# Optimization experiments

Measured on AMD Instinct MI355X. Metric: run time of the kernel, lower is better.

The kernel has to match this reference:

```python
import jax, jax.numpy as jnp
import numpy as np

H = W = 2048
TANH_C = 1.1486328125  # probability-correction constant from the model
DEG2RAD = np.float32(np.pi / 180.0)

# Fire-spread direction angle (degrees, East=0, counterclockwise) from the
# neighbor at 3x3 window position (r, c) toward the center cell.
DIR_DEG = jnp.array([[315., 270., 225.],
                     [  0.,   0., 180.],
                     [ 45.,  90., 135.]], dtype=jnp.float32)
CENTER_MASK = jnp.ones((3, 3), jnp.float32).at[1, 1].set(0.0)  # exclude self


def _neighborhood(x):
    """x: [H,W] -> [H,W,3,3] with [i,j,r,c] = x[i+r-1, j+c-1], zero padded."""
    xp = jnp.pad(x, 1)
    return jnp.stack(
        [jnp.stack([xp[r:r + H, c:c + W] for c in range(3)], axis=-1)
         for r in range(3)], axis=-2)


def setup_inputs() -> dict:
    key = jax.random.key(0)
    ks = jax.random.split(key, 8)
    p_veg = jax.random.uniform(ks[0], (H, W), jnp.float32)
    p_den = jax.random.uniform(ks[1], (H, W), jnp.float32)
    wind_velocity = jax.random.uniform(ks[2], (H, W), jnp.float32) * 10.0
    wind_towards_direction = jax.random.uniform(ks[3], (H, W), jnp.float32) * 360.0
    slope = (jax.random.uniform(ks[4], (H, W, 3, 3), jnp.float32) - 0.5) * 60.0
    burning = jax.random.uniform(ks[5], (H, W)) < 0.01  # sparse initial ignition
    burned = jnp.zeros((H, W), dtype=bool)
    rand_ignite = jax.random.uniform(ks[6], (H, W), jnp.float32)
    rand_continue = jax.random.uniform(ks[7], (H, W), jnp.float32)
    return dict(
        p_veg=p_veg, p_den=p_den,
        wind_velocity=wind_velocity, wind_towards_direction=wind_towards_direction,
        slope=slope,
        a=jnp.float32(0.1), p_h=jnp.float32(0.3),
        c_1=jnp.float32(0.1), c_2=jnp.float32(0.1), p_continue=jnp.float32(0.3),
        rand_ignite=rand_ignite, rand_continue=rand_continue,
        burning=burning, burned=burned,
    )


def reference(p_veg, p_den, wind_velocity, wind_towards_direction, slope,
              a, p_h, c_1, c_2, p_continue,
              rand_ignite, rand_continue, burning, burned):
    # p_w = exp(c1*V) * exp(c2*V*(cos(theta_w)-1)), theta_w = angle between
    # wind direction and per-neighbor spread direction. [H,W,3,3]
    theta_w = (wind_towards_direction[..., None, None] - DIR_DEG) * DEG2RAD
    p_w = (jnp.exp(c_1 * wind_velocity)[..., None, None]
           * jnp.exp(c_2 * wind_velocity[..., None, None] * (jnp.cos(theta_w) - 1.0)))
    # p_s = exp(a * theta_s), slope angle in radians. [H,W,3,3]
    p_s = jnp.exp(a * slope * DEG2RAD)
    # p_propagate = tanh(c * p_h*(1+p_veg)*(1+p_den)*p_w*p_s)
    p_base = p_h * (1.0 + p_veg) * (1.0 + p_den)  # [H,W]
    p_prop = jnp.tanh(TANH_C * (p_base[..., None, None] * p_w * p_s))
    # 8-neighbor burning indicators (center masked out). [H,W,3,3]
    nbr_burning = _neighborhood(burning.astype(jnp.float32)) * CENTER_MASK
    # p_ignite = 1 - prod_j (1 - p_propagate_j * burning_j)
    p_ignite = 1.0 - jnp.prod(1.0 - p_prop * nbr_burning, axis=(-2, -1))
    # Stochastic state transition.
    burnable = ~burning & ~burned
    new_ignited = burnable & (rand_ignite < p_ignite)
    keep = burning & (rand_continue < p_continue)
    new_burning = new_ignited | keep
    new_burned = burned | (burning & ~keep)
    return p_ignite, jnp.stack([new_burning, new_burned])
```

## Files before the change

### kernel.cpp

```cpp
#include <hip/hip_runtime.h>
#include <math.h>

namespace {

constexpr int H = 2048;
constexpr int W = 2048;
constexpr int HW = H * W;
constexpr int TR = 8;
constexpr int TC = 512;
constexpr int NTX = W / TC;
constexpr int NTY = H / TR;
constexpr int BPY = NTY / 8;

constexpr float TANH_C  = 1.1486328125f;
constexpr float DEG2RAD = 0.017453292519943295f;
constexpr float RT2H    = 0.70710678118654752f;
constexpr float LOG2E   = 1.4426950408889634f;
constexpr float TWOPI   = 6.283185307179586f;

__device__ __forceinline__ float fexp2(float x) {
#if __has_builtin(__builtin_amdgcn_exp2f)
    return __builtin_amdgcn_exp2f(x);
#else
    return __exp2f(x);
#endif
}
__device__ __forceinline__ float fcos_rev(float x) {
#if __has_builtin(__builtin_amdgcn_cosf)
    return __builtin_amdgcn_cosf(x);
#else
    return __cosf(x * TWOPI);
#endif
}
__device__ __forceinline__ float fsin_rev(float x) {
#if __has_builtin(__builtin_amdgcn_sinf)
    return __builtin_amdgcn_sinf(x);
#else
    return __sinf(x * TWOPI);
#endif
}
__device__ __forceinline__ float frcp(float x) {
#if __has_builtin(__builtin_amdgcn_rcpf)
    return __builtin_amdgcn_rcpf(x);
#else
    return 1.0f / x;
#endif
}

__global__ __launch_bounds__(256) void wildfire_step(
    const float* __restrict__ p_veg,  const float* __restrict__ p_den,
    const float* __restrict__ wind_v, const float* __restrict__ wind_d,
    const float* __restrict__ slope,
    const float* __restrict__ s_a,  const float* __restrict__ s_ph,
    const float* __restrict__ s_c1, const float* __restrict__ s_c2,
    const float* __restrict__ s_pc,
    const float* __restrict__ rand_ig, const float* __restrict__ rand_co,
    const int* __restrict__ burning, const int* __restrict__ burned,
    float* __restrict__ out)
{
    __shared__ __align__(16) float sb[TR + 2][520];
    __shared__ unsigned short q[TR * TC];
    __shared__ int qn;

    const int t = (int)threadIdx.x;
    const int g  = (int)blockIdx.y;
    const int ty = (g & 7) * BPY + (g >> 3);
    const int tx = (int)blockIdx.x;
    const int i0 = ty * TR;
    const int j0 = tx * TC;

    if (t == 0) qn = 0;

    for (int p = t; p < (TR + 2) * (TC / 4); p += 256) {
        const int r  = p >> 7;
        const int gq = p & 127;
        const int ii = i0 - 1 + r;
        int4 v = make_int4(0, 0, 0, 0);
        if (ii >= 0 && ii < H)
            v = *reinterpret_cast<const int4*>(burning + ii * W + j0 + 4 * gq);
        float4 f;
        f.x = v.x ? 1.f : 0.f;  f.y = v.y ? 1.f : 0.f;
        f.z = v.z ? 1.f : 0.f;  f.w = v.w ? 1.f : 0.f;
        *reinterpret_cast<float4*>(&sb[r][4 + 4 * gq]) = f;
    }
    if (t < TR + 2) {
        const int ii = i0 - 1 + t;
        sb[t][3] = (ii >= 0 && ii < H && j0 > 0)
                 ? (burning[ii * W + j0 - 1] ? 1.f : 0.f) : 0.f;
    } else if (t >= 64 && t < 64 + TR + 2) {
        const int r  = t - 64;
        const int ii = i0 - 1 + r;
        sb[r][4 + TC] = (ii >= 0 && ii < H && j0 + TC < W)
                 ? (burning[ii * W + j0 + TC] ? 1.f : 0.f) : 0.f;
    }
    __syncthreads();

    const float p_cont = s_pc[0];
#pragma unroll
    for (int k = 0; k < 4; ++k) {
        const int p   = t + (k << 8);
        const int row = p >> 7;
        const int jb  = (p & 127) * 4;
        const float4 a = *reinterpret_cast<const float4*>(&sb[row][4 + jb]);
        const float4 b = *reinterpret_cast<const float4*>(&sb[row + 1][4 + jb]);
        const float4 c = *reinterpret_cast<const float4*>(&sb[row + 2][4 + jb]);
        const float r0[6] = {sb[row][3 + jb],     a.x, a.y, a.z, a.w, sb[row][8 + jb]};
        const float r1[6] = {sb[row + 1][3 + jb], b.x, b.y, b.z, b.w, sb[row + 1][8 + jb]};
        const float r2[6] = {sb[row + 2][3 + jb], c.x, c.y, c.z, c.w, sb[row + 2][8 + jb]};

        bool isb[4];
#pragma unroll
        for (int x = 0; x < 4; ++x) {
            const float anyn = ((r0[x] + r0[x+1]) + (r0[x+2] + r1[x]))
                             + ((r1[x+2] + r2[x]) + (r2[x+1] + r2[x+2]));
            isb[x] = (r1[x+1] != 0.f);
            if (anyn != 0.f) {
                const int pos = atomicAdd(&qn, 1);
                q[pos] = (unsigned short)(row * TC + jb + x);
            }
        }

        const int gidx = (i0 + row) * W + j0 + jb;
        const int4 bd4 = *reinterpret_cast<const int4*>(burned + gidx);
        const int  bn[4] = {bd4.x, bd4.y, bd4.z, bd4.w};
        float rc[4] = {1.f, 1.f, 1.f, 1.f};
        if (isb[0] || isb[1] || isb[2] || isb[3]) {
            const float4 v = *reinterpret_cast<const float4*>(rand_co + gidx);
            rc[0] = v.x; rc[1] = v.y; rc[2] = v.z; rc[3] = v.w;
        }
        float4 o1, o2;
        float* o1p = &o1.x; float* o2p = &o2.x;
#pragma unroll
        for (int x = 0; x < 4; ++x) {
            const bool keep = isb[x] && (rc[x] < p_cont);
            o1p[x] = keep ? 1.f : 0.f;
            o2p[x] = ((bn[x] != 0) || (isb[x] && !keep)) ? 1.f : 0.f;
        }
        *reinterpret_cast<float4*>(out + gidx)          = make_float4(0.f, 0.f, 0.f, 0.f);
        *reinterpret_cast<float4*>(out + HW + gidx)     = o1;
        *reinterpret_cast<float4*>(out + 2 * HW + gidx) = o2;
    }
    __syncthreads();

    const int n = qn;
    const float a_  = s_a[0];
    const float p_h = s_ph[0];
    const float c1  = s_c1[0];
    const float c2  = s_c2[0];
    const float aslL = (a_ * DEG2RAD) * LOG2E;

    for (int k = t; k < n; k += 256) {
        const int cell = (int)q[k];
        const int row  = cell >> 9;
        const int col  = cell & 511;
        const int gidx = (i0 + row) * W + j0 + col;

        const float pv  = p_veg[gidx];
        const float pd  = p_den[gidx];
        const float wv  = wind_v[gidx];
        const float wd  = wind_d[gidx];
        const float rig = rand_ig[gidx];
        const int   bn  = burned[gidx];
        float sl[9];
        __builtin_memcpy(sl, slope + (size_t)gidx * 9, 9 * sizeof(float));

        const float b0 = sb[row][3+col],   b1 = sb[row][4+col],    b2 = sb[row][5+col];
        const float b3 = sb[row+1][3+col], bcn = sb[row+1][4+col], b5 = sb[row+1][5+col];
        const float b6 = sb[row+2][3+col], b7 = sb[row+2][4+col],  b8 = sb[row+2][5+col];
        const float cnt = ((b0 + b1) + (b2 + b3)) + ((b5 + b6) + (b7 + b8));

        const float wrev = wd * (1.f / 360.f);
        const float cw = fcos_rev(wrev);
        const float sw = fsin_rev(wrev);

        const float Lc2wv = (LOG2E * c2) * wv;
        const float cwv = Lc2wv * cw, swv = Lc2wv * sw;
        const float cwr = RT2H * cwv, swr = RT2H * swv;
        const float dpl = cwr + swr;
        const float dmi = cwr - swr;
        const float p_base = (p_h * (1.f + pv)) * (1.f + pd);
        const float Cz2 = (2.f * LOG2E * TANH_C) * p_base
                        * fexp2(LOG2E * (c1 * wv - c2 * wv));

#define NEIGHBOR(K, b, T, sv)                                            \
        const float q##K = fmaf(aslL, (sv), (T));                        \
        const float z##K = Cz2 * fexp2(q##K);                            \
        const float E##K = fexp2(z##K);                                  \
        const float d##K = fmaf((b), E##K, 1.f);

        NEIGHBOR(0, b0,  dmi, sl[0])
        NEIGHBOR(1, b1, -swv, sl[1])
        NEIGHBOR(2, b2, -dpl, sl[2])
        NEIGHBOR(3, b3,  cwv, sl[3])
        NEIGHBOR(5, b5, -cwv, sl[5])
        NEIGHBOR(6, b6,  dpl, sl[6])
        NEIGHBOR(7, b7,  swv, sl[7])
        NEIGHBOR(8, b8, -dmi, sl[8])
#undef NEIGHBOR
        const float den = ((d0 * d1) * (d2 * d3)) * ((d5 * d6) * (d7 * d8));
        const float num = fexp2(cnt);
        const float pig = fmaf(-num, frcp(den), 1.f);

        out[gidx] = pig;
        const bool ni = (bcn == 0.f) && (bn == 0) && (rig < pig);
        if (ni) out[HW + gidx] = 1.f;
    }
}

}

extern "C" void kernel_launch(void* const* d_in, const int* in_sizes, int n_in,
                              void* d_out, int out_size, void* d_ws, size_t ws_size,
                              hipStream_t stream)
{
    (void)in_sizes; (void)n_in; (void)out_size; (void)d_ws; (void)ws_size;
    dim3 grid(NTX, NTY, 1);
    dim3 block(256, 1, 1);
    hipLaunchKernelGGL(wildfire_step, grid, block, 0, stream,
        (const float*)d_in[0],  (const float*)d_in[1],
        (const float*)d_in[2],  (const float*)d_in[3],
        (const float*)d_in[4],
        (const float*)d_in[5],  (const float*)d_in[6],
        (const float*)d_in[7],  (const float*)d_in[8],
        (const float*)d_in[9],
        (const float*)d_in[10], (const float*)d_in[11],
        (const int*)d_in[12],   (const int*)d_in[13],
        (float*)d_out);
}
```

Baseline: 305.9 us.

## Replace LDS work queue with inline per-cell computation and dense prefetched loads

Removes the shared-memory compaction queue and second pass; each thread now prefetches all per-cell inputs with float4 loads up front and computes ignition probability inline only for cells with burning neighbors. Outputs are written once with coalesced vector stores instead of a zero-fill followed by scattered writes. This eliminates LDS atomics, a barrier and scattered gathers, but reads all input arrays in full regardless of sparsity, raises register pressure, and exposes wavefront divergence on the expensive path.

```diff
diff --git a/kernel.cpp b/kernel.cpp
--- a/kernel.cpp
+++ b/kernel.cpp
@@ -59,17 +59,32 @@
     float* __restrict__ out)
 {
     __shared__ __align__(16) float sb[TR + 2][520];
-    __shared__ unsigned short q[TR * TC];
-    __shared__ int qn;
-
-    const int t = (int)threadIdx.x;
+
+    const int t  = (int)threadIdx.x;
     const int g  = (int)blockIdx.y;
     const int ty = (g & 7) * BPY + (g >> 3);
     const int tx = (int)blockIdx.x;
     const int i0 = ty * TR;
     const int j0 = tx * TC;
 
-    if (t == 0) qn = 0;
+    float4 pv4[4], pd4[4], wv4[4], wd4[4], rg4[4], rc4[4];
+    int4   bd4[4];
+    int    gix[4];
+#pragma unroll
+    for (int k = 0; k < 4; ++k) {
+        const int p   = t + (k << 8);
+        const int row = p >> 7;
+        const int jb  = (p & 127) * 4;
+        const int gi  = (i0 + row) * W + j0 + jb;
+        gix[k] = gi;
+        pv4[k] = *reinterpret_cast<const float4*>(p_veg  + gi);
+        pd4[k] = *reinterpret_cast<const float4*>(p_den  + gi);
+        wv4[k] = *reinterpret_cast<const float4*>(wind_v + gi);
+        wd4[k] = *reinterpret_cast<const float4*>(wind_d + gi);
+        rg4[k] = *reinterpret_cast<const float4*>(rand_ig + gi);
+        rc4[k] = *reinterpret_cast<const float4*>(rand_co + gi);
+        bd4[k] = *reinterpret_cast<const int4*>(burned + gi);
+    }
 
     for (int p = t; p < (TR + 2) * (TC / 4); p += 256) {
         const int r  = p >> 7;
@@ -95,115 +110,95 @@
     }
     __syncthreads();
 
+    const float a_   = s_a[0];
+    const float p_h  = s_ph[0];
+    const float c1   = s_c1[0];
+    const float c2   = s_c2[0];
     const float p_cont = s_pc[0];
+    const float aslL = (a_ * DEG2RAD) * LOG2E;
+    const float CzK  = 2.f * LOG2E * TANH_C;
+
 #pragma unroll
     for (int k = 0; k < 4; ++k) {
         const int p   = t + (k << 8);
         const int row = p >> 7;
         const int jb  = (p & 127) * 4;
-        const float4 a = *reinterpret_cast<const float4*>(&sb[row][4 + jb]);
-        const float4 b = *reinterpret_cast<const float4*>(&sb[row + 1][4 + jb]);
-        const float4 c = *reinterpret_cast<const float4*>(&sb[row + 2][4 + jb]);
-        const float r0[6] = {sb[row][3 + jb],     a.x, a.y, a.z, a.w, sb[row][8 + jb]};
-        const float r1[6] = {sb[row + 1][3 + jb], b.x, b.y, b.z, b.w, sb[row + 1][8 + jb]};
-        const float r2[6] = {sb[row + 2][3 + jb], c.x, c.y, c.z, c.w, sb[row + 2][8 + jb]};
-
-        bool isb[4];
+        const float4 av = *reinterpret_cast<const float4*>(&sb[row][4 + jb]);
+        const float4 bv = *reinterpret_cast<const float4*>(&sb[row + 1][4 + jb]);
+        const float4 cv = *reinterpret_cast<const float4*>(&sb[row + 2][4 + jb]);
+        const float r0[6] = {sb[row][3 + jb],     av.x, av.y, av.z, av.w, sb[row][8 + jb]};
+        const float r1[6] = {sb[row + 1][3 + jb], bv.x, bv.y, bv.z, bv.w, sb[row + 1][8 + jb]};
+        const float r2[6] = {sb[row + 2][3 + jb], cv.x, cv.y, cv.z, cv.w, sb[row + 2][8 + jb]};
+
+        const float pv[4]  = {pv4[k].x, pv4[k].y, pv4[k].z, pv4[k].w};
+        const float pd[4]  = {pd4[k].x, pd4[k].y, pd4[k].z, pd4[k].w};
+        const float wv[4]  = {wv4[k].x, wv4[k].y, wv4[k].z, wv4[k].w};
+        const float wd[4]  = {wd4[k].x, wd4[k].y, wd4[k].z, wd4[k].w};
+        const float rg[4]  = {rg4[k].x, rg4[k].y, rg4[k].z, rg4[k].w};
+        const float rc[4]  = {rc4[k].x, rc4[k].y, rc4[k].z, rc4[k].w};
+        const int   bn[4]  = {bd4[k].x, bd4[k].y, bd4[k].z, bd4[k].w};
+
+        float4 o0, o1, o2;
+        float* o0p = &o0.x; float* o1p = &o1.x; float* o2p = &o2.x;
 #pragma unroll
         for (int x = 0; x < 4; ++x) {
             const float anyn = ((r0[x] + r0[x+1]) + (r0[x+2] + r1[x]))
                              + ((r1[x+2] + r2[x]) + (r2[x+1] + r2[x+2]));
-            isb[x] = (r1[x+1] != 0.f);
+            const bool isb = (r1[x+1] != 0.f);
+            float pig = 0.f;
+            bool  ni  = false;
+
             if (anyn != 0.f) {
-                const int pos = atomicAdd(&qn, 1);
-                q[pos] = (unsigned short)(row * TC + jb + x);
+                const int gidx = gix[k] + x;
+                float sl[9];
+                __builtin_memcpy(sl, slope + (size_t)gidx * 9, 9 * sizeof(float));
+
+                const float wrev = wd[x] * (1.f / 360.f);
+                const float cw = fcos_rev(wrev);
+                const float sw = fsin_rev(wrev);
+
+                const float Lc2wv = (LOG2E * c2) * wv[x];
+                const float cwv = Lc2wv * cw, swv = Lc2wv * sw;
+                const float cwr = RT2H * cwv, swr = RT2H * swv;
+                const float dpl = cwr + swr;
+                const float dmi = cwr - swr;
+                const float p_base = (p_h * (1.f + pv[x])) * (1.f + pd[x]);
+                const float Cz2 = CzK * p_base
+                                * fexp2(LOG2E * (c1 * wv[x] - c2 * wv[x]));
+
+#define NEIGHBOR(K, b, T, sv)                                            \
+                const float q##K = fmaf(aslL, (sv), (T));                \
+                const float z##K = Cz2 * fexp2(q##K);                    \
+                const float E##K = fexp2(z##K);                          \
+                const float d##K = fmaf((b), E##K, 1.f);
+
+                NEIGHBOR(0, r0[x],    dmi, sl[0])
+                NEIGHBOR(1, r0[x+1], -swv, sl[1])
+                NEIGHBOR(2, r0[x+2], -dpl, sl[2])
+                NEIGHBOR(3, r1[x],    cwv, sl[3])
+                NEIGHBOR(5, r1[x+2], -cwv, sl[5])
+                NEIGHBOR(6, r2[x],    dpl, sl[6])
+                NEIGHBOR(7, r2[x+1],  swv, sl[7])
+                NEIGHBOR(8, r2[x+2], -dmi, sl[8])
+#undef NEIGHBOR
+                const float den = ((d0 * d1) * (d2 * d3)) * ((d5 * d6) * (d7 * d8));
+                const float num = fexp2(anyn);
+                pig = fmaf(-num, frcp(den), 1.f);
+
+                ni = (!isb) && (bn[x] == 0) && (rg[x] < pig);
             }
+
+            const bool keep = isb && (rc[x] < p_cont);
+            const bool nb   = ni || keep;
+            const bool nd   = (bn[x] != 0) || (isb && !keep);
+            o0p[x] = pig;
+            o1p[x] = nb ? 1.f : 0.f;
+            o2p[x] = nd ? 1.f : 0.f;
         }
 
-        const int gidx = (i0 + row) * W + j0 + jb;
-        const int4 bd4 = *reinterpret_cast<const int4*>(burned + gidx);
-        const int  bn[4] = {bd4.x, bd4.y, bd4.z, bd4.w};
-        float rc[4] = {1.f, 1.f, 1.f, 1.f};
-        if (isb[0] || isb[1] || isb[2] || isb[3]) {
-            const float4 v = *reinterpret_cast<const float4*>(rand_co + gidx);
-            rc[0] = v.x; rc[1] = v.y; rc[2] = v.z; rc[3] = v.w;
-        }
-        float4 o1, o2;
-        float* o1p = &o1.x; float* o2p = &o2.x;
-#pragma unroll
-        for (int x = 0; x < 4; ++x) {
-            const bool keep = isb[x] && (rc[x] < p_cont);
-            o1p[x] = keep ? 1.f : 0.f;
-            o2p[x] = ((bn[x] != 0) || (isb[x] && !keep)) ? 1.f : 0.f;
-        }
-        *reinterpret_cast<float4*>(out + gidx)          = make_float4(0.f, 0.f, 0.f, 0.f);
-        *reinterpret_cast<float4*>(out + HW + gidx)     = o1;
-        *reinterpret_cast<float4*>(out + 2 * HW + gidx) = o2;
-    }
-    __syncthreads();
-
-    const int n = qn;
-    const float a_  = s_a[0];
-    const float p_h = s_ph[0];
-    const float c1  = s_c1[0];
-    const float c2  = s_c2[0];
-    const float aslL = (a_ * DEG2RAD) * LOG2E;
-
-    for (int k = t; k < n; k += 256) {
-        const int cell = (int)q[k];
-        const int row  = cell >> 9;
-        const int col  = cell & 511;
-        const int gidx = (i0 + row) * W + j0 + col;
-
-        const float pv  = p_veg[gidx];
-        const float pd  = p_den[gidx];
-        const float wv  = wind_v[gidx];
-        const float wd  = wind_d[gidx];
-        const float rig = rand_ig[gidx];
-        const int   bn  = burned[gidx];
-        float sl[9];
-        __builtin_memcpy(sl, slope + (size_t)gidx * 9, 9 * sizeof(float));
-
-        const float b0 = sb[row][3+col],   b1 = sb[row][4+col],    b2 = sb[row][5+col];
-        const float b3 = sb[row+1][3+col], bcn = sb[row+1][4+col], b5 = sb[row+1][5+col];
-        const float b6 = sb[row+2][3+col], b7 = sb[row+2][4+col],  b8 = sb[row+2][5+col];
-        const float cnt = ((b0 + b1) + (b2 + b3)) + ((b5 + b6) + (b7 + b8));
-
-        const float wrev = wd * (1.f / 360.f);
-        const float cw = fcos_rev(wrev);
-        const float sw = fsin_rev(wrev);
-
-        const float Lc2wv = (LOG2E * c2) * wv;
-        const float cwv = Lc2wv * cw, swv = Lc2wv * sw;
-        const float cwr = RT2H * cwv, swr = RT2H * swv;
-        const float dpl = cwr + swr;
-        const float dmi = cwr - swr;
-        const float p_base = (p_h * (1.f + pv)) * (1.f + pd);
-        const float Cz2 = (2.f * LOG2E * TANH_C) * p_base
-                        * fexp2(LOG2E * (c1 * wv - c2 * wv));
-
-#define NEIGHBOR(K, b, T, sv)                                            \
-        const float q##K = fmaf(aslL, (sv), (T));                        \
-        const float z##K = Cz2 * fexp2(q##K);                            \
-        const float E##K = fexp2(z##K);                                  \
-        const float d##K = fmaf((b), E##K, 1.f);
-
-        NEIGHBOR(0, b0,  dmi, sl[0])
-        NEIGHBOR(1, b1, -swv, sl[1])
-        NEIGHBOR(2, b2, -dpl, sl[2])
-        NEIGHBOR(3, b3,  cwv, sl[3])
-        NEIGHBOR(5, b5, -cwv, sl[5])
-        NEIGHBOR(6, b6,  dpl, sl[6])
-        NEIGHBOR(7, b7,  swv, sl[7])
-        NEIGHBOR(8, b8, -dmi, sl[8])
-#undef NEIGHBOR
-        const float den = ((d0 * d1) * (d2 * d3)) * ((d5 * d6) * (d7 * d8));
-        const float num = fexp2(cnt);
-        const float pig = fmaf(-num, frcp(den), 1.f);
-
-        out[gidx] = pig;
-        const bool ni = (bcn == 0.f) && (bn == 0) && (rig < pig);
-        if (ni) out[HW + gidx] = 1.f;
+        *reinterpret_cast<float4*>(out + gix[k])          = o0;
+        *reinterpret_cast<float4*>(out + HW + gix[k])     = o1;
+        *reinterpret_cast<float4*>(out + 2 * HW + gix[k]) = o2;
     }
 }
 
```

New measurement: 323.6 us. 5.8% more time.

## Replace shared-memory work queue with direct per-thread column processing on smaller tiles

Applied to the files above, without the earlier changes.

Drops the LDS atomic compaction queue and the second pass. Each thread now owns one column of a 4x256 tile and computes the ignition probability inline for any cell with a burning neighbor, then writes all three outputs once. This removes the atomics, the extra barrier and the zero-then-overwrite stores to out. In exchange, threads within a wavefront diverge wherever active cells are sparse, and loads become scalar (one float per thread) rather than float4.

```diff
diff --git a/kernel.cpp b/kernel.cpp
--- a/kernel.cpp
+++ b/kernel.cpp
@@ -6,10 +6,10 @@
 constexpr int H = 2048;
 constexpr int W = 2048;
 constexpr int HW = H * W;
-constexpr int TR = 8;
-constexpr int TC = 512;
-constexpr int NTX = W / TC;
-constexpr int NTY = H / TR;
+constexpr int TRr = 4;
+constexpr int TCc = 256;
+constexpr int NTX = W / TCc;
+constexpr int NTY = H / TRr;
 constexpr int BPY = NTY / 8;
 
 constexpr float TANH_C  = 1.1486328125f;
@@ -58,152 +58,126 @@
     const int* __restrict__ burning, const int* __restrict__ burned,
     float* __restrict__ out)
 {
-    __shared__ __align__(16) float sb[TR + 2][520];
-    __shared__ unsigned short q[TR * TC];
-    __shared__ int qn;
-
-    const int t = (int)threadIdx.x;
+    __shared__ __align__(16) float sb[TRr + 2][264];
+
+    const int t  = (int)threadIdx.x;
     const int g  = (int)blockIdx.y;
     const int ty = (g & 7) * BPY + (g >> 3);
-    const int tx = (int)blockIdx.x;
-    const int i0 = ty * TR;
-    const int j0 = tx * TC;
-
-    if (t == 0) qn = 0;
-
-    for (int p = t; p < (TR + 2) * (TC / 4); p += 256) {
-        const int r  = p >> 7;
-        const int gq = p & 127;
+    const int i0 = ty * TRr;
+    const int j0 = (int)blockIdx.x * TCc;
+
+    for (int p = t; p < (TRr + 2) * (TCc / 4); p += 256) {
+        const int r  = p >> 6;
+        const int qd = p & 63;
         const int ii = i0 - 1 + r;
         int4 v = make_int4(0, 0, 0, 0);
         if (ii >= 0 && ii < H)
-            v = *reinterpret_cast<const int4*>(burning + ii * W + j0 + 4 * gq);
+            v = *reinterpret_cast<const int4*>(burning + ii * W + j0 + 4 * qd);
         float4 f;
         f.x = v.x ? 1.f : 0.f;  f.y = v.y ? 1.f : 0.f;
         f.z = v.z ? 1.f : 0.f;  f.w = v.w ? 1.f : 0.f;
-        *reinterpret_cast<float4*>(&sb[r][4 + 4 * gq]) = f;
-    }
-    if (t < TR + 2) {
+        *reinterpret_cast<float4*>(&sb[r][4 + 4 * qd]) = f;
+    }
+    if (t < TRr + 2) {
         const int ii = i0 - 1 + t;
         sb[t][3] = (ii >= 0 && ii < H && j0 > 0)
                  ? (burning[ii * W + j0 - 1] ? 1.f : 0.f) : 0.f;
-    } else if (t >= 64 && t < 64 + TR + 2) {
+    } else if (t >= 64 && t < 64 + TRr + 2) {
         const int r  = t - 64;
         const int ii = i0 - 1 + r;
-        sb[r][4 + TC] = (ii >= 0 && ii < H && j0 + TC < W)
-                 ? (burning[ii * W + j0 + TC] ? 1.f : 0.f) : 0.f;
+        sb[r][4 + TCc] = (ii >= 0 && ii < H && j0 + TCc < W)
+                 ? (burning[ii * W + j0 + TCc] ? 1.f : 0.f) : 0.f;
     }
     __syncthreads();
 
+    const float a_     = s_a[0];
+    const float p_h    = s_ph[0];
+    const float c1     = s_c1[0];
+    const float c2     = s_c2[0];
     const float p_cont = s_pc[0];
+    const float aslL   = (a_ * DEG2RAD) * LOG2E;
+    const float CzK    = 2.f * LOG2E * TANH_C;
+
+    float anyn[TRr], bcn[TRr];
+    int   bn[TRr];
 #pragma unroll
-    for (int k = 0; k < 4; ++k) {
-        const int p   = t + (k << 8);
-        const int row = p >> 7;
-        const int jb  = (p & 127) * 4;
-        const float4 a = *reinterpret_cast<const float4*>(&sb[row][4 + jb]);
-        const float4 b = *reinterpret_cast<const float4*>(&sb[row + 1][4 + jb]);
-        const float4 c = *reinterpret_cast<const float4*>(&sb[row + 2][4 + jb]);
-        const float r0[6] = {sb[row][3 + jb],     a.x, a.y, a.z, a.w, sb[row][8 + jb]};
-        const float r1[6] = {sb[row + 1][3 + jb], b.x, b.y, b.z, b.w, sb[row + 1][8 + jb]};
-        const float r2[6] = {sb[row + 2][3 + jb], c.x, c.y, c.z, c.w, sb[row + 2][8 + jb]};
-
-        bool isb[4];
+    for (int x = 0; x < TRr; ++x) {
+        const float b0 = sb[x][t + 3],     b1 = sb[x][t + 4],     b2 = sb[x][t + 5];
+        const float b3 = sb[x + 1][t + 3], bc = sb[x + 1][t + 4], b5 = sb[x + 1][t + 5];
+        const float b6 = sb[x + 2][t + 3], b7 = sb[x + 2][t + 4], b8 = sb[x + 2][t + 5];
+        anyn[x] = ((b0 + b1) + (b2 + b3)) + ((b5 + b6) + (b7 + b8));
+        bcn[x]  = bc;
+        bn[x]   = burned[(i0 + x) * W + j0 + t];
+    }
+
+    float pig[TRr];
+    bool  ni[TRr];
 #pragma unroll
-        for (int x = 0; x < 4; ++x) {
-            const float anyn = ((r0[x] + r0[x+1]) + (r0[x+2] + r1[x]))
-                             + ((r1[x+2] + r2[x]) + (r2[x+1] + r2[x+2]));
-            isb[x] = (r1[x+1] != 0.f);
-            if (anyn != 0.f) {
-                const int pos = atomicAdd(&qn, 1);
-                q[pos] = (unsigned short)(row * TC + jb + x);
-            }
+    for (int x = 0; x < TRr; ++x) {
+        pig[x] = 0.f;
+        ni[x]  = false;
+        if (anyn[x] != 0.f) {
+            const int gidx = (i0 + x) * W + j0 + t;
+            const float pv  = p_veg[gidx];
+            const float pd  = p_den[gidx];
+            const float wv  = wind_v[gidx];
+            const float wd  = wind_d[gidx];
+            const float rig = rand_ig[gidx];
+            float sl[9];
+            __builtin_memcpy(sl, slope + (size_t)gidx * 9, 9 * sizeof(float));
+
+            const float b0 = sb[x][t + 3],     b1 = sb[x][t + 4],     b2 = sb[x][t + 5];
+            const float b3 = sb[x + 1][t + 3],                        b5 = sb[x + 1][t + 5];
+            const float b6 = sb[x + 2][t + 3], b7 = sb[x + 2][t + 4], b8 = sb[x + 2][t + 5];
+
+            const float wrev = wd * (1.f / 360.f);
+            const float cw = fcos_rev(wrev);
+            const float sw = fsin_rev(wrev);
+
+            const float Lc2wv = (LOG2E * c2) * wv;
+            const float cwv = Lc2wv * cw, swv = Lc2wv * sw;
+            const float cwr = RT2H * cwv, swr = RT2H * swv;
+            const float dpl = cwr + swr;
+            const float dmi = cwr - swr;
+            const float p_base = (p_h * (1.f + pv)) * (1.f + pd);
+            const float Cz2 = CzK * p_base
+                            * fexp2(LOG2E * (c1 * wv - c2 * wv));
+
+#define NEIGHBOR(K, b, T, sv)                                            \
+            const float q##K = fmaf(aslL, (sv), (T));                    \
+            const float z##K = Cz2 * fexp2(q##K);                        \
+            const float E##K = fexp2(z##K);                              \
+            const float d##K = fmaf((b), E##K, 1.f);
+
+            NEIGHBOR(0, b0,  dmi, sl[0])
+            NEIGHBOR(1, b1, -swv, sl[1])
+            NEIGHBOR(2, b2, -dpl, sl[2])
+            NEIGHBOR(3, b3,  cwv, sl[3])
+            NEIGHBOR(5, b5, -cwv, sl[5])
+            NEIGHBOR(6, b6,  dpl, sl[6])
+            NEIGHBOR(7, b7,  swv, sl[7])
+            NEIGHBOR(8, b8, -dmi, sl[8])
+#undef NEIGHBOR
+            const float den = ((d0 * d1) * (d2 * d3)) * ((d5 * d6) * (d7 * d8));
+            const float num = fexp2(anyn[x]);
+            pig[x] = fmaf(-num, frcp(den), 1.f);
+
+            ni[x] = (bcn[x] == 0.f) && (bn[x] == 0) && (rig < pig[x]);
         }
-
-        const int gidx = (i0 + row) * W + j0 + jb;
-        const int4 bd4 = *reinterpret_cast<const int4*>(burned + gidx);
-        const int  bn[4] = {bd4.x, bd4.y, bd4.z, bd4.w};
-        float rc[4] = {1.f, 1.f, 1.f, 1.f};
-        if (isb[0] || isb[1] || isb[2] || isb[3]) {
-            const float4 v = *reinterpret_cast<const float4*>(rand_co + gidx);
-            rc[0] = v.x; rc[1] = v.y; rc[2] = v.z; rc[3] = v.w;
-        }
-        float4 o1, o2;
-        float* o1p = &o1.x; float* o2p = &o2.x;
+    }
+
 #pragma unroll
-        for (int x = 0; x < 4; ++x) {
-            const bool keep = isb[x] && (rc[x] < p_cont);
-            o1p[x] = keep ? 1.f : 0.f;
-            o2p[x] = ((bn[x] != 0) || (isb[x] && !keep)) ? 1.f : 0.f;
-        }
-        *reinterpret_cast<float4*>(out + gidx)          = make_float4(0.f, 0.f, 0.f, 0.f);
-        *reinterpret_cast<float4*>(out + HW + gidx)     = o1;
-        *reinterpret_cast<float4*>(out + 2 * HW + gidx) = o2;
-    }
-    __syncthreads();
-
-    const int n = qn;
-    const float a_  = s_a[0];
-    const float p_h = s_ph[0];
-    const float c1  = s_c1[0];
-    const float c2  = s_c2[0];
-    const float aslL = (a_ * DEG2RAD) * LOG2E;
-
-    for (int k = t; k < n; k += 256) {
-        const int cell = (int)q[k];
-        const int row  = cell >> 9;
-        const int col  = cell & 511;
-        const int gidx = (i0 + row) * W + j0 + col;
-
-        const float pv  = p_veg[gidx];
-        const float pd  = p_den[gidx];
-        const float wv  = wind_v[gidx];
-        const float wd  = wind_d[gidx];
-        const float rig = rand_ig[gidx];
-        const int   bn  = burned[gidx];
-        float sl[9];
-        __builtin_memcpy(sl, slope + (size_t)gidx * 9, 9 * sizeof(float));
-
-        const float b0 = sb[row][3+col],   b1 = sb[row][4+col],    b2 = sb[row][5+col];
-        const float b3 = sb[row+1][3+col], bcn = sb[row+1][4+col], b5 = sb[row+1][5+col];
-        const float b6 = sb[row+2][3+col], b7 = sb[row+2][4+col],  b8 = sb[row+2][5+col];
-        const float cnt = ((b0 + b1) + (b2 + b3)) + ((b5 + b6) + (b7 + b8));
-
-        const float wrev = wd * (1.f / 360.f);
-        const float cw = fcos_rev(wrev);
-        const float sw = fsin_rev(wrev);
-
-        const float Lc2wv = (LOG2E * c2) * wv;
-        const float cwv = Lc2wv * cw, swv = Lc2wv * sw;
-        const float cwr = RT2H * cwv, swr = RT2H * swv;
-        const float dpl = cwr + swr;
-        const float dmi = cwr - swr;
-        const float p_base = (p_h * (1.f + pv)) * (1.f + pd);
-        const float Cz2 = (2.f * LOG2E * TANH_C) * p_base
-                        * fexp2(LOG2E * (c1 * wv - c2 * wv));
-
-#define NEIGHBOR(K, b, T, sv)                                            \
-        const float q##K = fmaf(aslL, (sv), (T));                        \
-        const float z##K = Cz2 * fexp2(q##K);                            \
-        const float E##K = fexp2(z##K);                                  \
-        const float d##K = fmaf((b), E##K, 1.f);
-
-        NEIGHBOR(0, b0,  dmi, sl[0])
-        NEIGHBOR(1, b1, -swv, sl[1])
-        NEIGHBOR(2, b2, -dpl, sl[2])
-        NEIGHBOR(3, b3,  cwv, sl[3])
-        NEIGHBOR(5, b5, -cwv, sl[5])
-        NEIGHBOR(6, b6,  dpl, sl[6])
-        NEIGHBOR(7, b7,  swv, sl[7])
-        NEIGHBOR(8, b8, -dmi, sl[8])
-#undef NEIGHBOR
-        const float den = ((d0 * d1) * (d2 * d3)) * ((d5 * d6) * (d7 * d8));
-        const float num = fexp2(cnt);
-        const float pig = fmaf(-num, frcp(den), 1.f);
-
-        out[gidx] = pig;
-        const bool ni = (bcn == 0.f) && (bn == 0) && (rig < pig);
-        if (ni) out[HW + gidx] = 1.f;
+    for (int x = 0; x < TRr; ++x) {
+        const int  gidx = (i0 + x) * W + j0 + t;
+        const bool isb  = (bcn[x] != 0.f);
+        float rcv = 1.f;
+        if (isb) rcv = rand_co[gidx];
+        const bool keep = isb && (rcv < p_cont);
+        const bool nb   = ni[x] || keep;
+        const bool nd   = (bn[x] != 0) || (isb && !keep);
+        out[gidx]          = pig[x];
+        out[HW + gidx]     = nb ? 1.f : 0.f;
+        out[2 * HW + gidx] = nd ? 1.f : 0.f;
     }
 }
 
```

Result: no change. 304.5 us (-0.5%).
